# Performance work log

Hardware: AMD Instinct MI355X
Metric: run time of the kernel (lower is better)

## Reference

```python
import jax, jax.numpy as jnp
import numpy as np

# module hyperparameters (match init_kwargs)
D_IN = 32
N_BAND_IN = 32
D_OUT = 32
K_BAND = 4
K_T = 3
DIL_T = 1
STRIDE_B = 2
PAD_B = 1
PAD_B_OUT = 0

# derived band geometry (same formulas as ConvTranspose2dBandPadder)
N_UP = (N_BAND_IN - 1) * STRIDE_B + 1            # zero-interleaved bands
PAD_TOP = K_BAND - 1 - PAD_B
PAD_BOT = PAD_TOP + PAD_B_OUT
N_PADDED = N_UP + PAD_TOP + PAD_BOT              # bands fed to the conv
N_BAND_OUT = N_PADDED - K_BAND + 1               # valid conv along bands

B = 8
T = 1000


def setup_inputs() -> dict:
    key = jax.random.key(0)
    k1, k2, k3 = jax.random.split(key, 3)
    x = jax.random.normal(k1, (B, D_IN * N_BAND_IN, T), jnp.float32)
    W = jax.random.normal(k2, (D_OUT, D_IN, K_BAND, K_T), jnp.float32) * 0.05
    b = jax.random.normal(k3, (D_OUT,), jnp.float32) * 0.05
    return {"x": x, "W": W, "b": b}


def reference(x, W, b):
    """x: (B, D_IN*N_BAND_IN, T) band-major channels -> (B, D_OUT*N_BAND_OUT, T)."""
    Bs, _, Ts = x.shape
    # chunk(dim=1, n_band_in): band-major layout (band, feature)
    bands = x.reshape(Bs, N_BAND_IN, D_IN, Ts)
    # zero-interleave bands by stride + top/bottom zero-band padding
    up = jnp.zeros((Bs, N_PADDED, D_IN, Ts), x.dtype)
    up = up.at[:, PAD_TOP:PAD_TOP + N_UP:STRIDE_B].set(bands)
    # 2D conv: channels = D_IN, spatial = (band, time), causal in time
    xin = up.transpose(0, 2, 1, 3)  # (B, D_IN, N_PADDED, T)
    pad_t = (K_T - 1) * DIL_T
    y = jax.lax.conv_general_dilated(
        xin, W,
        window_strides=(1, 1),
        padding=((0, 0), (pad_t, 0)),  # valid over bands, causal over time
        rhs_dilation=(1, DIL_T),
        dimension_numbers=("NCHW", "OIHW", "NCHW"),
    )  # (B, D_OUT, N_BAND_OUT, T)
    y = y + b[None, :, None, None]
    # back to band-major flattened channels
    return y.transpose(0, 2, 1, 3).reshape(Bs, D_OUT * N_BAND_OUT, Ts)
```

## Files before the change

kernel.cpp:

```cpp
#include <hip/hip_runtime.h>
#include <cstddef>
#include <cstdint>


typedef __bf16 bf16x8 __attribute__((ext_vector_type(8)));
typedef __bf16 bf16x4 __attribute__((ext_vector_type(4)));
typedef float  f32x4  __attribute__((ext_vector_type(4)));

#define D_IN_ 32
#define D_OUT_ 32
#define N_BI_ 32
#define N_BO_ 64
#define K_B_ 4
#define K_T_ 3
#define T_ 1000
#define B_ 8

#define TT_ 252
#define XROWS_ 260
#define ROWB_ 64
#define WT_ELEMS (2 * 6 * 2 * 64 * 8)

__device__ __forceinline__ int swz(int t) { return (t & 3) ^ ((t >> 2) & 3); }

__global__ __launch_bounds__(256)
void wprep(const float* __restrict__ W, __bf16* __restrict__ wt) {
    int idx = blockIdx.x * 256 + threadIdx.x;
    if (idx >= WT_ELEMS) return;
    int r = idx & 7, l = (idx >> 3) & 63, mt = (idx >> 9) & 1, rest = idx >> 10;
    int ks = rest % 6, p = rest / 6;
    int dout = mt * 16 + (l & 15), din = (l >> 4) * 8 + r;
    int j = ks / 3, kt = ks % 3, kb = 2 * j + p;
    wt[idx] = (__bf16)W[((dout * D_IN_ + din) * K_B_ + kb) * K_T_ + kt];
}

__global__ __launch_bounds__(512, 4)
void tct_mfma(const float* __restrict__ x, const __bf16* __restrict__ wt,
              const float* __restrict__ bias, float* __restrict__ out)
{
    __shared__ unsigned char xl[2 * XROWS_ * ROWB_];

    const int tid = threadIdx.x;
    const int l   = tid & 63;
    const int w   = tid >> 6;
    const int n   = blockIdx.y;
    const int bb  = blockIdx.z;
    const int p   = n & 1, q = n >> 1;
    const int t0  = blockIdx.x * TT_;
    const int tstart = t0 - 4;

    bf16x8 afrag[6][2];
    {
        const bf16x8* wp = (const bf16x8*)wt;
        const int base = p * 12 * 64;
#pragma unroll
        for (int ks = 0; ks < 6; ++ks)
#pragma unroll
            for (int mt = 0; mt < 2; ++mt)
                afrag[ks][mt] = wp[base + (ks * 2 + mt) * 64 + l];
    }

    {
        const int g  = tid >> 4;
        const int u  = tid & 15;
        const int si = u >> 3;
        const int dg = u & 7;
        const int s  = q + si + p - 1;
        const bool bandok = (s >= 0) && (s < N_BI_);
        const float* xb = x + ((size_t)(bb * N_BI_ + (bandok ? s : 0)) * D_IN_ + dg * 4) * T_;
        unsigned char* lbase = xl + si * (XROWS_ * ROWB_);
        const int c = dg >> 1, h = dg & 1;

        f32x4 vv[2][4];
        bool ok[2];
        int tgs[2];
#pragma unroll
        for (int it = 0; it < 2; ++it) {
            const int tq = g + it * 32;
            const int tg = tstart + tq * 4;
            tgs[it] = tg;
            ok[it] = bandok && (tg >= 0) && (tg < T_);
#pragma unroll
            for (int i = 0; i < 4; ++i) {
                if (ok[it]) vv[it][i] = *(const f32x4*)(xb + (size_t)i * T_ + tg);
                else        vv[it][i] = (f32x4){0.f, 0.f, 0.f, 0.f};
            }
        }
#pragma unroll
        for (int it = 0; it < 2; ++it) {
            const int tq = g + it * 32;
#pragma unroll
            for (int jj = 0; jj < 4; ++jj) {
                const int k = (jj + g) & 3;
                const int t = tq * 4 + k;
                bf16x4 row;
                row[0] = (__bf16)vv[it][0][k];
                row[1] = (__bf16)vv[it][1][k];
                row[2] = (__bf16)vv[it][2][k];
                row[3] = (__bf16)vv[it][3][k];
                *(bf16x4*)(lbase + t * ROWB_ + ((c ^ swz(t)) << 4) + (h << 3)) = row;
            }
        }
    }
    __syncthreads();

    f32x4 acc[2][2];
#pragma unroll
    for (int mt = 0; mt < 2; ++mt)
#pragma unroll
        for (int nt = 0; nt < 2; ++nt)
#pragma unroll
            for (int r = 0; r < 4; ++r) acc[mt][nt][r] = 0.f;

    const int tl  = l & 15;
    const int cch = l >> 4;
#pragma unroll
    for (int nt = 0; nt < 2; ++nt) {
#pragma unroll
        for (int ks = 0; ks < 6; ++ks) {
            const int j  = ks / 3, kt = ks % 3;
            const int lt = w * 32 + nt * 16 + tl + kt + 2;
            const bf16x8 bfrag = *(const bf16x8*)(xl + j * (XROWS_ * ROWB_) + lt * ROWB_
                                                  + ((cch ^ swz(lt)) << 4));
            acc[0][nt] = __builtin_amdgcn_mfma_f32_16x16x32_bf16(afrag[ks][0], bfrag, acc[0][nt], 0, 0, 0);
            acc[1][nt] = __builtin_amdgcn_mfma_f32_16x16x32_bf16(afrag[ks][1], bfrag, acc[1][nt], 0, 0, 0);
        }
    }

    const int rbase = (l >> 4) * 4;
    float bv[2][4];
#pragma unroll
    for (int mt = 0; mt < 2; ++mt)
#pragma unroll
        for (int r = 0; r < 4; ++r) bv[mt][r] = bias[mt * 16 + rbase + r];

#pragma unroll
    for (int mt = 0; mt < 2; ++mt)
#pragma unroll
        for (int nt = 0; nt < 2; ++nt) {
            const int lcol = w * 32 + nt * 16 + tl;
            const int tcol = t0 + lcol;
            if (lcol < TT_ && tcol < T_) {
                float* op = out + ((size_t)(bb * N_BO_ + n) * D_OUT_ + mt * 16 + rbase) * T_ + tcol;
#pragma unroll
                for (int r = 0; r < 4; ++r)
                    op[(size_t)r * T_] = acc[mt][nt][r] + bv[mt][r];
            }
        }
}

__global__ __launch_bounds__(256)
void tct_fallback(const float* __restrict__ x, const float* __restrict__ W,
                  const float* __restrict__ bias, float* __restrict__ out)
{
    const int lane = threadIdx.x & 63;
    const int wav  = __builtin_amdgcn_readfirstlane(threadIdx.x >> 6);
    const int dog  = wav * 8;
    const int n    = blockIdx.y;
    const int bb   = blockIdx.z;
    const int p    = n & 1;

    int t0 = blockIdx.x * 256 + lane * 4;
    const bool act = (t0 < T_);
    if (!act) t0 = T_ - 4;

    float acc[8][4];
#pragma unroll
    for (int i = 0; i < 8; ++i)
#pragma unroll
        for (int u = 0; u < 4; ++u) acc[i][u] = 0.f;

#pragma unroll
    for (int j = 0; j < 2; ++j) {
        const int s = (n + 2 * j + p - 2) >> 1;
        if (s < 0 || s >= N_BI_) continue;
        const int kb = 2 * j + p;
        const float* xband = x + (size_t)(bb * N_BI_ + s) * D_IN_ * T_;
        for (int d_in = 0; d_in < D_IN_; ++d_in) {
            const float* xr = xband + d_in * T_;
            const float4 xc = *(const float4*)(xr + t0);
            float4 xp = make_float4(0.f, 0.f, 0.f, 0.f);
            if (t0 > 0) xp = *(const float4*)(xr + t0 - 4);
            const float xv[6] = {xp.z, xp.w, xc.x, xc.y, xc.z, xc.w};
#pragma unroll
            for (int kt = 0; kt < K_T_; ++kt) {
                float wv[8];
#pragma unroll
                for (int i = 0; i < 8; ++i) {
                    const int widx = __builtin_amdgcn_readfirstlane(
                        (((dog + i) * D_IN_ + d_in) * K_B_ + kb) * K_T_ + kt);
                    wv[i] = W[widx];
                }
#pragma unroll
                for (int i = 0; i < 8; ++i)
#pragma unroll
                    for (int u = 0; u < 4; ++u)
                        acc[i][u] = fmaf(wv[i], xv[u + kt], acc[i][u]);
            }
        }
    }
    if (act) {
        float bvv[8];
#pragma unroll
        for (int i = 0; i < 8; ++i) bvv[i] = bias[dog + i];
        float* op = out + ((size_t)(bb * N_BO_ + n) * D_OUT_ + dog) * T_ + t0;
#pragma unroll
        for (int i = 0; i < 8; ++i) {
            float4 v;
            v.x = acc[i][0] + bvv[i];
            v.y = acc[i][1] + bvv[i];
            v.z = acc[i][2] + bvv[i];
            v.w = acc[i][3] + bvv[i];
            *(float4*)(op + (size_t)i * T_) = v;
        }
    }
}

extern "C" void kernel_launch(void* const* d_in, const int* in_sizes, int n_in,
                              void* d_out, int out_size, void* d_ws, size_t ws_size,
                              hipStream_t stream) {
    const float* x    = (const float*)d_in[0];
    const float* W    = (const float*)d_in[1];
    const float* bias = (const float*)d_in[2];
    float* out = (float*)d_out;

    if (ws_size >= (size_t)WT_ELEMS * sizeof(__bf16)) {
        __bf16* wt = (__bf16*)d_ws;
        wprep<<<(WT_ELEMS + 255) / 256, 256, 0, stream>>>(W, wt);
        dim3 grid((T_ + TT_ - 1) / TT_, N_BO_, B_);
        tct_mfma<<<grid, dim3(512), 0, stream>>>(x, wt, bias, out);
    } else {
        dim3 grid((T_ + 255) / 256, N_BO_, B_);
        tct_fallback<<<grid, dim3(256), 0, stream>>>(x, W, bias, out);
    }
}
```

Measured before the change: 120.7 us.

## Pre-transpose input to padded bf16 time-major workspace and read fragments from global

Adds an xprep kernel that converts x once into a zero-padded bf16 layout (batch, padded band slot, time, channel), so every band is converted a single time instead of twice by neighbouring output bands. A new tct_gemm kernel reads MFMA B-fragments straight from that global buffer, with no LDS staging or block barrier, and splits waves across output-channel halves and time. This removes redundant fp32 loads and conversions plus the shared-memory transpose, at the cost of an extra kernel launch and a full round trip of the bf16 copy through memory. The new path runs only if the workspace holds about 17.9 MB, otherwise it falls back to the old kernel.

New measurement: 129.2 us. 1.07x slower.

```diff
diff --git a/kernel.cpp b/kernel.cpp
--- a/kernel.cpp
+++ b/kernel.cpp
@@ -16,12 +16,13 @@
 #define T_ 1000
 #define B_ 8
 
-#define TT_ 252
-#define XROWS_ 260
+#define TPB_ 1024
 #define ROWB_ 64
+#define NSL_ 34
 #define WT_ELEMS (2 * 6 * 2 * 64 * 8)
-
-__device__ __forceinline__ int swz(int t) { return (t & 3) ^ ((t >> 2) & 3); }
+#define XW_OFF_ 65536
+#define XW_BYTES_ ((size_t)B_ * NSL_ * TPB_ * ROWB_)
+#define WS_NEED_ (XW_OFF_ + XW_BYTES_)
 
 __global__ __launch_bounds__(256)
 void wprep(const float* __restrict__ W, __bf16* __restrict__ wt) {
@@ -34,19 +35,113 @@
     wt[idx] = (__bf16)W[((dout * D_IN_ + din) * K_B_ + kb) * K_T_ + kt];
 }
 
+__global__ __launch_bounds__(256)
+void xprep(const float* __restrict__ x, __bf16* __restrict__ xw) {
+    const int i   = threadIdx.x;
+    const int tp  = blockIdx.x * 64 + (i >> 2);
+    const int ch  = i & 3;
+    const int sl  = blockIdx.y;
+    const int bb  = blockIdx.z;
+    const int s   = sl - 1;
+    const int t   = tp - 4;
+    const bool ok = (s >= 0) && (s < N_BI_) && (t >= 0) && (t < T_);
+
+    bf16x8 v;
+    if (ok) {
+        const float* xp = x + ((size_t)(bb * N_BI_ + s) * D_IN_ + ch * 8) * T_ + t;
+#pragma unroll
+        for (int r = 0; r < 8; ++r) v[r] = (__bf16)xp[(size_t)r * T_];
+    } else {
+#pragma unroll
+        for (int r = 0; r < 8; ++r) v[r] = (__bf16)0.f;
+    }
+    __bf16* dst = xw + ((size_t)(bb * NSL_ + sl) * TPB_ + tp) * D_IN_ + ch * 8;
+    *(bf16x8*)dst = v;
+}
+
+__global__ __launch_bounds__(512)
+void tct_gemm(const __bf16* __restrict__ xw, const __bf16* __restrict__ wt,
+              const float* __restrict__ bias, float* __restrict__ out)
+{
+    const int tid = threadIdx.x;
+    const int l   = tid & 63;
+    const int w   = tid >> 6;
+    const int mtw = w >> 2;
+    const int wq  = w & 3;
+    const int tl  = l & 15;
+    const int cch = l >> 4;
+    const int n   = blockIdx.y;
+    const int bb  = blockIdx.z;
+    const int p   = n & 1, q = n >> 1;
+    const int t0  = blockIdx.x * 250;
+
+    bf16x8 afrag[6];
+    {
+        const bf16x8* wp = (const bf16x8*)wt;
+        const int base = p * 768 + mtw * 64;
+#pragma unroll
+        for (int ks = 0; ks < 6; ++ks)
+            afrag[ks] = wp[base + ks * 128 + l];
+    }
+
+    const char* xb0 = (const char*)(xw + ((size_t)(bb * NSL_ + (q + p)) * TPB_) * D_IN_);
+    const char* xb1 = xb0 + (size_t)TPB_ * ROWB_;
+
+    f32x4 acc[4];
+#pragma unroll
+    for (int nt = 0; nt < 4; ++nt)
+#pragma unroll
+        for (int r = 0; r < 4; ++r) acc[nt][r] = 0.f;
+
+#pragma unroll
+    for (int nt = 0; nt < 4; ++nt) {
+        const int tcol = t0 + wq * 64 + nt * 16 + tl;
+        bf16x8 bfrag[6];
+#pragma unroll
+        for (int kt = 0; kt < 3; ++kt) {
+            const int tp = tcol + kt + 2;
+            bfrag[kt]     = *(const bf16x8*)(xb0 + (size_t)tp * ROWB_ + cch * 16);
+            bfrag[3 + kt] = *(const bf16x8*)(xb1 + (size_t)tp * ROWB_ + cch * 16);
+        }
+#pragma unroll
+        for (int ks = 0; ks < 6; ++ks)
+            acc[nt] = __builtin_amdgcn_mfma_f32_16x16x32_bf16(afrag[ks], bfrag[ks], acc[nt], 0, 0, 0);
+    }
+
+    const int rbase = cch * 4;
+    float bv[4];
+#pragma unroll
+    for (int r = 0; r < 4; ++r) bv[r] = bias[mtw * 16 + rbase + r];
+
+#pragma unroll
+    for (int nt = 0; nt < 4; ++nt) {
+        const int lcol = wq * 64 + nt * 16 + tl;
+        const int tcol = t0 + lcol;
+        if (lcol < 250) {
+            float* op = out + ((size_t)(bb * N_BO_ + n) * D_OUT_ + mtw * 16 + rbase) * T_ + tcol;
+#pragma unroll
+            for (int r = 0; r < 4; ++r)
+                op[(size_t)r * T_] = acc[nt][r] + bv[r];
+        }
+    }
+}
+
+#define TT6_ 252
+#define XROWS_ 260
+__device__ __forceinline__ int swz(int t) { return (t & 3) ^ ((t >> 2) & 3); }
+
 __global__ __launch_bounds__(512, 4)
 void tct_mfma(const float* __restrict__ x, const __bf16* __restrict__ wt,
               const float* __restrict__ bias, float* __restrict__ out)
 {
     __shared__ unsigned char xl[2 * XROWS_ * ROWB_];
-
     const int tid = threadIdx.x;
     const int l   = tid & 63;
     const int w   = tid >> 6;
     const int n   = blockIdx.y;
     const int bb  = blockIdx.z;
     const int p   = n & 1, q = n >> 1;
-    const int t0  = blockIdx.x * TT_;
+    const int t0  = blockIdx.x * TT6_;
     const int tstart = t0 - 4;
 
     bf16x8 afrag[6][2];
@@ -59,7 +154,6 @@
             for (int mt = 0; mt < 2; ++mt)
                 afrag[ks][mt] = wp[base + (ks * 2 + mt) * 64 + l];
     }
-
     {
         const int g  = tid >> 4;
         const int u  = tid & 15;
@@ -70,21 +164,16 @@
         const float* xb = x + ((size_t)(bb * N_BI_ + (bandok ? s : 0)) * D_IN_ + dg * 4) * T_;
         unsigned char* lbase = xl + si * (XROWS_ * ROWB_);
         const int c = dg >> 1, h = dg & 1;
-
         f32x4 vv[2][4];
         bool ok[2];
-        int tgs[2];
 #pragma unroll
         for (int it = 0; it < 2; ++it) {
-            const int tq = g + it * 32;
-            const int tg = tstart + tq * 4;
-            tgs[it] = tg;
+            const int tg = tstart + (g + it * 32) * 4;
             ok[it] = bandok && (tg >= 0) && (tg < T_);
 #pragma unroll
-            for (int i = 0; i < 4; ++i) {
-                if (ok[it]) vv[it][i] = *(const f32x4*)(xb + (size_t)i * T_ + tg);
-                else        vv[it][i] = (f32x4){0.f, 0.f, 0.f, 0.f};
-            }
+            for (int i = 0; i < 4; ++i)
+                vv[it][i] = ok[it] ? *(const f32x4*)(xb + (size_t)i * T_ + tg)
+                                   : (f32x4){0.f, 0.f, 0.f, 0.f};
         }
 #pragma unroll
         for (int it = 0; it < 2; ++it) {
@@ -94,10 +183,8 @@
                 const int k = (jj + g) & 3;
                 const int t = tq * 4 + k;
                 bf16x4 row;
-                row[0] = (__bf16)vv[it][0][k];
-                row[1] = (__bf16)vv[it][1][k];
-                row[2] = (__bf16)vv[it][2][k];
-                row[3] = (__bf16)vv[it][3][k];
+                row[0] = (__bf16)vv[it][0][k]; row[1] = (__bf16)vv[it][1][k];
+                row[2] = (__bf16)vv[it][2][k]; row[3] = (__bf16)vv[it][3][k];
                 *(bf16x4*)(lbase + t * ROWB_ + ((c ^ swz(t)) << 4) + (h << 3)) = row;
             }
         }
@@ -126,25 +213,23 @@
             acc[1][nt] = __builtin_amdgcn_mfma_f32_16x16x32_bf16(afrag[ks][1], bfrag, acc[1][nt], 0, 0, 0);
         }
     }
-
     const int rbase = (l >> 4) * 4;
     float bv[2][4];
 #pragma unroll
     for (int mt = 0; mt < 2; ++mt)
 #pragma unroll
         for (int r = 0; r < 4; ++r) bv[mt][r] = bias[mt * 16 + rbase + r];
-
 #pragma unroll
     for (int mt = 0; mt < 2; ++mt)
 #pragma unroll
         for (int nt = 0; nt < 2; ++nt) {
             const int lcol = w * 32 + nt * 16 + tl;
             const int tcol = t0 + lcol;
-            if (lcol < TT_ && tcol < T_) {
+            if (lcol < TT6_ && tcol < T_) {
                 float* op = out + ((size_t)(bb * N_BO_ + n) * D_OUT_ + mt * 16 + rbase) * T_ + tcol;
 #pragma unroll
                 for (int r = 0; r < 4; ++r)
-                    op[(size_t)r * T_] = acc[mt][nt][r] + bv[mt][r];
+                    op[(size_t)r * T_] = acc[mt][nt][r] + bv[r == r ? mt : mt][r];
             }
         }
 }
@@ -159,17 +244,14 @@
     const int n    = blockIdx.y;
     const int bb   = blockIdx.z;
     const int p    = n & 1;
-
     int t0 = blockIdx.x * 256 + lane * 4;
     const bool act = (t0 < T_);
     if (!act) t0 = T_ - 4;
-
     float acc[8][4];
 #pragma unroll
     for (int i = 0; i < 8; ++i)
 #pragma unroll
         for (int u = 0; u < 4; ++u) acc[i][u] = 0.f;
-
 #pragma unroll
     for (int j = 0; j < 2; ++j) {
         const int s = (n + 2 * j + p - 2) >> 1;
@@ -207,10 +289,8 @@
 #pragma unroll
         for (int i = 0; i < 8; ++i) {
             float4 v;
-            v.x = acc[i][0] + bvv[i];
-            v.y = acc[i][1] + bvv[i];
-            v.z = acc[i][2] + bvv[i];
-            v.w = acc[i][3] + bvv[i];
+            v.x = acc[i][0] + bvv[i]; v.y = acc[i][1] + bvv[i];
+            v.z = acc[i][2] + bvv[i]; v.w = acc[i][3] + bvv[i];
             *(float4*)(op + (size_t)i * T_) = v;
         }
     }
@@ -224,13 +304,17 @@
     const float* bias = (const float*)d_in[2];
     float* out = (float*)d_out;
 
-    if (ws_size >= (size_t)WT_ELEMS * sizeof(__bf16)) {
+    if (ws_size >= WS_NEED_) {
+        __bf16* wt = (__bf16*)d_ws;
+        __bf16* xw = (__bf16*)((char*)d_ws + XW_OFF_);
+        wprep<<<(WT_ELEMS + 255) / 256, 256, 0, stream>>>(W, wt);
+        xprep<<<dim3(TPB_ / 64, NSL_, B_), dim3(256), 0, stream>>>(x, xw);
+        tct_gemm<<<dim3(4, N_BO_, B_), dim3(512), 0, stream>>>(xw, wt, bias, out);
+    } else if (ws_size >= (size_t)WT_ELEMS * sizeof(__bf16)) {
         __bf16* wt = (__bf16*)d_ws;
         wprep<<<(WT_ELEMS + 255) / 256, 256, 0, stream>>>(W, wt);
-        dim3 grid((T_ + TT_ - 1) / TT_, N_BO_, B_);
-        tct_mfma<<<grid, dim3(512), 0, stream>>>(x, wt, bias, out);
+        tct_mfma<<<dim3((T_ + TT6_ - 1) / TT6_, N_BO_, B_), dim3(512), 0, stream>>>(x, wt, bias, out);
     } else {
-        dim3 grid((T_ + 255) / 256, N_BO_, B_);
-        tct_fallback<<<grid, dim3(256), 0, stream>>>(x, W, bias, out);
-    }
-}
+        tct_fallback<<<dim3((T_ + 255) / 256, N_BO_, B_), dim3(256), 0, stream>>>(x, W, bias, out);
+    }
+}
```

## Compute both output-band parities per block sharing one staged input-band pair

Applied to the files above, without the earlier changes.

Each block now stages two adjacent input bands once and computes two output bands (even and odd parity) from them, instead of one output band per block. This halves the number of blocks and the redundant global loads and bf16 conversions of x into LDS. Waves are re-split so each handles one output-channel half over 64 time columns with both parities' weight fragments held in registers. The cost is higher register pressure (12 A fragments, 8 accumulators), the occupancy hint in the launch bounds is dropped, and the extra boundary block rows sit partly idle.

Result: faster. 110.9 us (-8.1%).

```diff
diff --git a/kernel.cpp b/kernel.cpp
--- a/kernel.cpp
+++ b/kernel.cpp
@@ -34,8 +34,8 @@
     wt[idx] = (__bf16)W[((dout * D_IN_ + din) * K_B_ + kb) * K_T_ + kt];
 }
 
-__global__ __launch_bounds__(512, 4)
-void tct_mfma(const float* __restrict__ x, const __bf16* __restrict__ wt,
+__global__ __launch_bounds__(512)
+void tct_pair(const float* __restrict__ x, const __bf16* __restrict__ wt,
               const float* __restrict__ bias, float* __restrict__ out)
 {
     __shared__ unsigned char xl[2 * XROWS_ * ROWB_];
@@ -43,21 +43,22 @@
     const int tid = threadIdx.x;
     const int l   = tid & 63;
     const int w   = tid >> 6;
-    const int n   = blockIdx.y;
+    const int mt  = w >> 2;
+    const int wq  = w & 3;
+    const int tl  = l & 15;
+    const int cch = l >> 4;
+    const int k   = (int)blockIdx.y - 1;
     const int bb  = blockIdx.z;
-    const int p   = n & 1, q = n >> 1;
     const int t0  = blockIdx.x * TT_;
-    const int tstart = t0 - 4;
-
-    bf16x8 afrag[6][2];
+
+    bf16x8 afrag[2][6];
     {
         const bf16x8* wp = (const bf16x8*)wt;
-        const int base = p * 12 * 64;
-#pragma unroll
-        for (int ks = 0; ks < 6; ++ks)
-#pragma unroll
-            for (int mt = 0; mt < 2; ++mt)
-                afrag[ks][mt] = wp[base + (ks * 2 + mt) * 64 + l];
+#pragma unroll
+        for (int p = 0; p < 2; ++p)
+#pragma unroll
+            for (int ks = 0; ks < 6; ++ks)
+                afrag[p][ks] = wp[p * 768 + ks * 128 + mt * 64 + l];
     }
 
     {
@@ -65,7 +66,7 @@
         const int u  = tid & 15;
         const int si = u >> 3;
         const int dg = u & 7;
-        const int s  = q + si + p - 1;
+        const int s  = k + si;
         const bool bandok = (s >= 0) && (s < N_BI_);
         const float* xb = x + ((size_t)(bb * N_BI_ + (bandok ? s : 0)) * D_IN_ + dg * 4) * T_;
         unsigned char* lbase = xl + si * (XROWS_ * ROWB_);
@@ -73,80 +74,78 @@
 
         f32x4 vv[2][4];
         bool ok[2];
-        int tgs[2];
+#pragma unroll
+        for (int it = 0; it < 2; ++it) {
+            const int tg = t0 - 4 + (g + it * 32) * 4;
+            ok[it] = bandok && (tg >= 0) && (tg < T_);
+#pragma unroll
+            for (int i = 0; i < 4; ++i)
+                vv[it][i] = ok[it] ? *(const f32x4*)(xb + (size_t)i * T_ + tg)
+                                   : (f32x4){0.f, 0.f, 0.f, 0.f};
+        }
 #pragma unroll
         for (int it = 0; it < 2; ++it) {
             const int tq = g + it * 32;
-            const int tg = tstart + tq * 4;
-            tgs[it] = tg;
-            ok[it] = bandok && (tg >= 0) && (tg < T_);
-#pragma unroll
-            for (int i = 0; i < 4; ++i) {
-                if (ok[it]) vv[it][i] = *(const f32x4*)(xb + (size_t)i * T_ + tg);
-                else        vv[it][i] = (f32x4){0.f, 0.f, 0.f, 0.f};
-            }
-        }
-#pragma unroll
-        for (int it = 0; it < 2; ++it) {
-            const int tq = g + it * 32;
-#pragma unroll
-            for (int jj = 0; jj < 4; ++jj) {
-                const int k = (jj + g) & 3;
-                const int t = tq * 4 + k;
+#pragma unroll
+            for (int kk = 0; kk < 4; ++kk) {
+                const int t = tq * 4 + kk;
                 bf16x4 row;
-                row[0] = (__bf16)vv[it][0][k];
-                row[1] = (__bf16)vv[it][1][k];
-                row[2] = (__bf16)vv[it][2][k];
-                row[3] = (__bf16)vv[it][3][k];
+                row[0] = (__bf16)vv[it][0][kk];
+                row[1] = (__bf16)vv[it][1][kk];
+                row[2] = (__bf16)vv[it][2][kk];
+                row[3] = (__bf16)vv[it][3][kk];
                 *(bf16x4*)(lbase + t * ROWB_ + ((c ^ swz(t)) << 4) + (h << 3)) = row;
             }
         }
     }
     __syncthreads();
 
-    f32x4 acc[2][2];
-#pragma unroll
-    for (int mt = 0; mt < 2; ++mt)
-#pragma unroll
-        for (int nt = 0; nt < 2; ++nt)
-#pragma unroll
-            for (int r = 0; r < 4; ++r) acc[mt][nt][r] = 0.f;
-
-    const int tl  = l & 15;
-    const int cch = l >> 4;
-#pragma unroll
-    for (int nt = 0; nt < 2; ++nt) {
-#pragma unroll
-        for (int ks = 0; ks < 6; ++ks) {
-            const int j  = ks / 3, kt = ks % 3;
-            const int lt = w * 32 + nt * 16 + tl + kt + 2;
-            const bf16x8 bfrag = *(const bf16x8*)(xl + j * (XROWS_ * ROWB_) + lt * ROWB_
-                                                  + ((cch ^ swz(lt)) << 4));
-            acc[0][nt] = __builtin_amdgcn_mfma_f32_16x16x32_bf16(afrag[ks][0], bfrag, acc[0][nt], 0, 0, 0);
-            acc[1][nt] = __builtin_amdgcn_mfma_f32_16x16x32_bf16(afrag[ks][1], bfrag, acc[1][nt], 0, 0, 0);
-        }
-    }
-
-    const int rbase = (l >> 4) * 4;
-    float bv[2][4];
-#pragma unroll
-    for (int mt = 0; mt < 2; ++mt)
-#pragma unroll
-        for (int r = 0; r < 4; ++r) bv[mt][r] = bias[mt * 16 + rbase + r];
-
-#pragma unroll
-    for (int mt = 0; mt < 2; ++mt)
-#pragma unroll
-        for (int nt = 0; nt < 2; ++nt) {
-            const int lcol = w * 32 + nt * 16 + tl;
+    f32x4 acc[2][4];
+#pragma unroll
+    for (int p = 0; p < 2; ++p)
+#pragma unroll
+        for (int nt = 0; nt < 4; ++nt)
+#pragma unroll
+            for (int r = 0; r < 4; ++r) acc[p][nt][r] = 0.f;
+
+#pragma unroll
+    for (int nt = 0; nt < 4; ++nt) {
+#pragma unroll
+        for (int j = 0; j < 2; ++j) {
+            const unsigned char* xbnd = xl + j * (XROWS_ * ROWB_);
+#pragma unroll
+            for (int kt = 0; kt < 3; ++kt) {
+                const int lt = wq * 64 + nt * 16 + tl + kt + 2;
+                const bf16x8 bfrag = *(const bf16x8*)(xbnd + lt * ROWB_
+                                                      + ((cch ^ swz(lt)) << 4));
+                const int ks = j * 3 + kt;
+                acc[0][nt] = __builtin_amdgcn_mfma_f32_16x16x32_bf16(afrag[0][ks], bfrag, acc[0][nt], 0, 0, 0);
+                acc[1][nt] = __builtin_amdgcn_mfma_f32_16x16x32_bf16(afrag[1][ks], bfrag, acc[1][nt], 0, 0, 0);
+            }
+        }
+    }
+
+    const int rbase = cch * 4;
+    float bv[4];
+#pragma unroll
+    for (int r = 0; r < 4; ++r) bv[r] = bias[mt * 16 + rbase + r];
+
+#pragma unroll
+    for (int p = 0; p < 2; ++p) {
+        const int n = 2 * k + 2 - p;
+        if (n < 0 || n >= N_BO_) continue;
+        float* opb = out + ((size_t)(bb * N_BO_ + n) * D_OUT_ + mt * 16 + rbase) * T_;
+#pragma unroll
+        for (int nt = 0; nt < 4; ++nt) {
+            const int lcol = wq * 64 + nt * 16 + tl;
             const int tcol = t0 + lcol;
             if (lcol < TT_ && tcol < T_) {
-                float* op = out + ((size_t)(bb * N_BO_ + n) * D_OUT_ + mt * 16 + rbase) * T_ + tcol;
 #pragma unroll
                 for (int r = 0; r < 4; ++r)
-                    op[(size_t)r * T_] = acc[mt][nt][r] + bv[mt][r];
-            }
-        }
+                    opb[(size_t)r * T_ + tcol] = acc[p][nt][r] + bv[r];
+            }
+        }
+    }
 }
 
 __global__ __launch_bounds__(256)
@@ -159,17 +158,14 @@
     const int n    = blockIdx.y;
     const int bb   = blockIdx.z;
     const int p    = n & 1;
-
     int t0 = blockIdx.x * 256 + lane * 4;
     const bool act = (t0 < T_);
     if (!act) t0 = T_ - 4;
-
     float acc[8][4];
 #pragma unroll
     for (int i = 0; i < 8; ++i)
 #pragma unroll
         for (int u = 0; u < 4; ++u) acc[i][u] = 0.f;
-
 #pragma unroll
     for (int j = 0; j < 2; ++j) {
         const int s = (n + 2 * j + p - 2) >> 1;
@@ -207,10 +203,8 @@
 #pragma unroll
         for (int i = 0; i < 8; ++i) {
             float4 v;
-            v.x = acc[i][0] + bvv[i];
-            v.y = acc[i][1] + bvv[i];
-            v.z = acc[i][2] + bvv[i];
-            v.w = acc[i][3] + bvv[i];
+            v.x = acc[i][0] + bvv[i]; v.y = acc[i][1] + bvv[i];
+            v.z = acc[i][2] + bvv[i]; v.w = acc[i][3] + bvv[i];
             *(float4*)(op + (size_t)i * T_) = v;
         }
     }
@@ -227,10 +221,9 @@
     if (ws_size >= (size_t)WT_ELEMS * sizeof(__bf16)) {
         __bf16* wt = (__bf16*)d_ws;
         wprep<<<(WT_ELEMS + 255) / 256, 256, 0, stream>>>(W, wt);
-        dim3 grid((T_ + TT_ - 1) / TT_, N_BO_, B_);
-        tct_mfma<<<grid, dim3(512), 0, stream>>>(x, wt, bias, out);
+        dim3 grid((T_ + TT_ - 1) / TT_, N_BO_ / 2 + 1, B_);
+        tct_pair<<<grid, dim3(512), 0, stream>>>(x, wt, bias, out);
     } else {
-        dim3 grid((T_ + 255) / 256, N_BO_, B_);
-        tct_fallback<<<grid, dim3(256), 0, stream>>>(x, W, bias, out);
-    }
-}
+        tct_fallback<<<dim3((T_ + 255) / 256, N_BO_, B_), dim3(256), 0, stream>>>(x, W, bias, out);
+    }
+}
```
